# Kernel optimization log

Hardware: AMD Instinct MI355X
Metric: run time of the kernel (lower is better)

## Reference

```python
import jax, jax.numpy as jnp
import numpy as np

B, S, DIM = 2, 2048, 4096
NH, NKV, HD = 32, 8, 128
N_REP = NH // NKV


def setup_inputs() -> dict:
    key = jax.random.key(0)
    ks = jax.random.split(key, 6)
    scale = 0.02
    x = jax.random.normal(ks[0], (B, S, DIM), dtype=jnp.float32)
    # RoPE table: angles[s, i] = s / 10000^(2i/HD); stored as (cos, sin) pairs
    inv_freq = 1.0 / (10000.0 ** (np.arange(0, HD, 2, dtype=np.float32) / HD))
    ang = np.arange(S, dtype=np.float32)[:, None] * inv_freq[None, :]  # [S, HD/2]
    freqs_cis = jnp.asarray(np.stack([np.cos(ang), np.sin(ang)], axis=-1), dtype=jnp.float32)
    wq = jax.random.normal(ks[1], (DIM, NH * HD), dtype=jnp.float32) * scale
    wk = jax.random.normal(ks[2], (DIM, NKV * HD), dtype=jnp.float32) * scale
    wv = jax.random.normal(ks[3], (DIM, NKV * HD), dtype=jnp.float32) * scale
    wo = jax.random.normal(ks[4], (NH * HD, DIM), dtype=jnp.float32) * scale
    return {"x": x, "freqs_cis": freqs_cis, "wq": wq, "wk": wk, "wv": wv, "wo": wo}


def _apply_rope(xh, fc):
    # xh: [B, S, H, HD]; fc: [S, HD/2, 2] (cos, sin). Pairs are consecutive dims
    # (matches torch view_as_complex on reshape(..., -1, 2)). Done in fp32.
    b, s, h, d = xh.shape
    xp = xh.astype(jnp.float32).reshape(b, s, h, d // 2, 2)
    cos = fc[:, None, :, 0]  # [S, 1, HD/2] -> broadcasts over batch & heads
    sin = fc[:, None, :, 1]
    xr, xi = xp[..., 0], xp[..., 1]
    out_r = xr * cos - xi * sin
    out_i = xr * sin + xi * cos
    return jnp.stack([out_r, out_i], axis=-1).reshape(b, s, h, d).astype(xh.dtype)


def reference(x, freqs_cis, wq, wk, wv, wo):
    b, s, _ = x.shape
    xq = (x @ wq).reshape(b, s, NH, HD)
    xk = (x @ wk).reshape(b, s, NKV, HD)
    xv = (x @ wv).reshape(b, s, NKV, HD)
    xq = _apply_rope(xq, freqs_cis)
    xk = _apply_rope(xk, freqs_cis)
    new_k, new_v = xk, xv  # kv_cache is None -> new cache is this step's K/V

    # GQA: group query heads [NH] as [NKV, N_REP]; no K/V materialized repeat.
    q = xq.transpose(0, 2, 1, 3).reshape(b, NKV, N_REP, s, HD)
    k = xk.transpose(0, 2, 1, 3)  # [B, NKV, S, HD]
    v = xv.transpose(0, 2, 1, 3)
    scores = jnp.einsum("bgrqd,bgkd->bgrqk", q, k) / jnp.sqrt(jnp.float32(HD))
    attn = jax.nn.softmax(scores, axis=-1)  # is_causal=False -> full attention
    ctx = jnp.einsum("bgrqk,bgkd->bgrqd", attn, v)  # [B, NKV, N_REP, S, HD]
    ctx = ctx.reshape(b, NH, s, HD).transpose(0, 2, 1, 3).reshape(b, s, NH * HD)
    out = ctx @ wo
    return out, new_k, new_v
```

## Files before the change

### kernel.cpp

```cpp
#include <hip/hip_runtime.h>
#include <hip/hip_bf16.h>
#include <math.h>

#define B_    2
#define S_    2048
#define DIM_  4096
#define NH_   32
#define NKV_  8
#define HD_   128
#define NREP_ 4

typedef __attribute__((ext_vector_type(8))) short bf16x8;
typedef __attribute__((ext_vector_type(4))) float floatx4;

__device__ __forceinline__ unsigned short f2bf(float f) {
    unsigned int u = __float_as_uint(f);
    unsigned int r = (u + 0x7FFFu + ((u >> 16) & 1u)) >> 16;
    return (unsigned short)r;
}
__device__ __forceinline__ float bf2f(unsigned short u) {
    return __uint_as_float((unsigned int)u << 16);
}
__device__ __forceinline__ void gload_lds16(const unsigned short* g, unsigned short* l) {
    __builtin_amdgcn_global_load_lds(
        (const __attribute__((address_space(1))) void*)g,
        (__attribute__((address_space(3))) void*)l, 16, 0, 0);
}

__global__ __launch_bounds__(256)
void convert_bf16(const float* __restrict__ in, unsigned short* __restrict__ out,
                  long long n) {
    long long i = ((long long)blockIdx.x * 256 + threadIdx.x) * 4;
    if (i >= n) return;
    const float4 v = *(const float4*)(in + i);
    ushort4 o;
    o.x = f2bf(v.x); o.y = f2bf(v.y); o.z = f2bf(v.z); o.w = f2bf(v.w);
    *(ushort4*)(out + i) = o;
}

__global__ __launch_bounds__(256)
void transpose_conv(const float* __restrict__ W, unsigned short* __restrict__ Wt,
                    int K, int N) {
    __shared__ unsigned short t[32][33];
    const int tx = threadIdx.x & 31, ty = threadIdx.x >> 5;
    const int n0 = blockIdx.x * 32, k0 = blockIdx.y * 32;
    for (int i = 0; i < 4; ++i)
        t[ty + i * 8][tx] = f2bf(W[(size_t)(k0 + ty + i * 8) * N + n0 + tx]);
    __syncthreads();
    for (int i = 0; i < 4; ++i)
        Wt[(size_t)(n0 + ty + i * 8) * K + k0 + tx] = t[tx][ty + i * 8];
}

template<bool OUT_BF16>
__global__ __launch_bounds__(256)
void gemm_bt(const unsigned short* __restrict__ A,
             const unsigned short* __restrict__ Bt,
             void* __restrict__ C, int M, int N, int K) {
    __shared__ unsigned short As[128 * 32];
    __shared__ unsigned short Bs[128 * 32];
    const int tid  = threadIdx.x;
    const int lane = tid & 63;
    const int wave = tid >> 6;
    const int l16  = lane & 15;
    const int quad = lane >> 4;
    const int tileM = blockIdx.x * 128, tileN = blockIdx.y * 128;
    const int waveM = (wave >> 1) * 64, waveN = (wave & 1) * 64;

    floatx4 acc[4][4] = {};

    const int r0 = tid >> 2, ko = (tid & 3) * 8;

    for (int k0 = 0; k0 < K; k0 += 32) {
        for (int p = 0; p < 2; ++p) {
            const int idx = p * 256 + tid;
            const int row = r0 + p * 64;
            gload_lds16(A  + (size_t)(tileM + row) * K + k0 + ko, &As[idx * 8]);
            gload_lds16(Bt + (size_t)(tileN + row) * K + k0 + ko, &Bs[idx * 8]);
        }
        __syncthreads();
        bf16x8 af[4], bfr[4];
        for (int i = 0; i < 4; ++i) {
            af[i]  = *(const bf16x8*)&As[(waveM + i * 16 + l16) * 32 + quad * 8];
            bfr[i] = *(const bf16x8*)&Bs[(waveN + i * 16 + l16) * 32 + quad * 8];
        }
        for (int mi = 0; mi < 4; ++mi)
            for (int ni = 0; ni < 4; ++ni)
                acc[mi][ni] = __builtin_amdgcn_mfma_f32_16x16x32_bf16(
                    af[mi], bfr[ni], acc[mi][ni], 0, 0, 0);
        __syncthreads();
    }
    for (int mi = 0; mi < 4; ++mi)
        for (int r = 0; r < 4; ++r) {
            const int row = tileM + waveM + mi * 16 + quad * 4 + r;
            for (int ni = 0; ni < 4; ++ni) {
                const int col = tileN + waveN + ni * 16 + l16;
                if (OUT_BF16)
                    ((unsigned short*)C)[(size_t)row * N + col] = f2bf(acc[mi][ni][r]);
                else
                    ((float*)C)[(size_t)row * N + col] = acc[mi][ni][r];
            }
        }
}

__global__ __launch_bounds__(256)
void rope2(unsigned short* __restrict__ qio, const float* __restrict__ xk,
           const float* __restrict__ nv, const float* __restrict__ fc,
           unsigned short* __restrict__ kb, unsigned short* __restrict__ vtb,
           float* __restrict__ new_k) {
    const long long QP = (long long)B_ * S_ * NH_ * (HD_ / 2);
    const long long KP = (long long)B_ * S_ * NKV_ * (HD_ / 2);
    const long long idx = (long long)blockIdx.x * 256 + threadIdx.x;
    if (idx < QP) {
        const int d2 = (int)(idx & 63);
        const long long rh = idx >> 6;
        const int s = (int)((rh / NH_) % S_);
        const ushort2 u = *(const ushort2*)(qio + idx * 2);
        const float xr = bf2f(u.x), xi = bf2f(u.y);
        const float cs = fc[((size_t)s * 64 + d2) * 2];
        const float sn = fc[((size_t)s * 64 + d2) * 2 + 1];
        *(ushort2*)(qio + idx * 2) =
            make_ushort2(f2bf(xr * cs - xi * sn), f2bf(xr * sn + xi * cs));
    } else if (idx < QP + KP) {
        const long long e = idx - QP;
        const int d2 = (int)(e & 63);
        const long long rh = e >> 6;
        const int g = (int)(rh & (NKV_ - 1));
        const long long row = rh >> 3;
        const int b = (int)(row / S_), s = (int)(row % S_);
        const float2 v = *(const float2*)(xk + e * 2);
        const float cs = fc[((size_t)s * 64 + d2) * 2];
        const float sn = fc[((size_t)s * 64 + d2) * 2 + 1];
        const float orr = v.x * cs - v.y * sn;
        const float oii = v.x * sn + v.y * cs;
        *(float2*)(new_k + e * 2) = make_float2(orr, oii);
        const size_t kbi = ((size_t)(b * NKV_ + g) * S_ + s) * HD_ + d2 * 2;
        *(ushort2*)(kb + kbi) = make_ushort2(f2bf(orr), f2bf(oii));
    } else if (idx < QP + 2 * KP) {
        const long long e = idx - QP - KP;
        const float2 v = *(const float2*)(nv + e * 2);
        const long long fe = e * 2;
        const int c = (int)(fe & (HD_ - 1));
        const long long rh = fe >> 7;
        const int g = (int)(rh & (NKV_ - 1));
        const long long row = rh >> 3;
        const int b = (int)(row / S_), s = (int)(row % S_);
        const size_t base = ((size_t)(b * NKV_ + g) * HD_ + c) * S_ + s;
        vtb[base]      = f2bf(v.x);
        vtb[base + S_] = f2bf(v.y);
    }
}

__global__ __launch_bounds__(256)
void flash_attn(const unsigned short* __restrict__ qb,
                const unsigned short* __restrict__ kb,
                const unsigned short* __restrict__ vtb,
                unsigned short* __restrict__ ctxb) {
    __shared__ unsigned short Ks[2][64 * 128];
    __shared__ unsigned short Vs[2][128 * 64];
    __shared__ unsigned short Plds[4][16 * 72];
    const int tid  = threadIdx.x;
    const int wave = tid >> 6, lane = tid & 63;
    const int l16  = lane & 15, quad = lane >> 4;
    const int bi  = blockIdx.x;
    const int qt4 = bi & (S_ / 64 - 1);
    const int bh  = bi >> 5;
    const int h = bh & (NH_ - 1), b = bh >> 5;
    const int g = h >> 2;
    const int qt = qt4 * 4 + wave;
    const float scale = 0.08838834764831845f;

    const unsigned short* kbase = kb  + (size_t)(b * NKV_ + g) * S_ * HD_;
    const unsigned short* vbase = vtb + (size_t)(b * NKV_ + g) * HD_ * S_;

    bf16x8 qf[4];
    {
        const unsigned short* qp =
            qb + ((size_t)(b * S_ + qt * 16 + l16) * NH_ + h) * HD_;
        for (int c = 0; c < 4; ++c) qf[c] = *(const bf16x8*)(qp + c * 32 + quad * 8);
    }

    float m_i[4], l_i[4];
    for (int r = 0; r < 4; ++r) { m_i[r] = -1e30f; l_i[r] = 0.f; }
    floatx4 oacc[8] = {};
    unsigned short* pw = &Plds[wave][0];

    auto stage = [&](int buf, int kt) {
        for (int rnd = 0; rnd < 4; ++rnd) {
            const int ci = rnd * 256 + tid;
            const int row = ci >> 4, c = ci & 15;
            gload_lds16(kbase + (size_t)(kt + row) * HD_ + (c ^ (row & 15)) * 8,
                        &Ks[buf][ci * 8]);
        }
        for (int rnd = 0; rnd < 4; ++rnd) {
            const int ci = rnd * 256 + tid;
            const int row = ci >> 3, c = ci & 7;
            gload_lds16(vbase + (size_t)row * S_ + kt + (c ^ (row & 7)) * 8,
                        &Vs[buf][ci * 8]);
        }
    };

    stage(0, 0);
    __syncthreads();

    int cur = 0;
    for (int kt = 0; kt < S_; kt += 64) {
        if (kt + 64 < S_) stage(cur ^ 1, kt + 64);
        floatx4 sacc[4] = {};
        for (int t = 0; t < 4; ++t) {
            const int row = t * 16 + l16;
            const char* kp = (const char*)&Ks[cur][row * 128];
            for (int c = 0; c < 4; ++c) {
                const bf16x8 kf = *(const bf16x8*)
                    (kp + ((c * 64 + quad * 16) ^ (l16 << 4)));
                sacc[t] = __builtin_amdgcn_mfma_f32_16x16x32_bf16(qf[c], kf, sacc[t], 0, 0, 0);
            }
        }
        float alpha[4];
        for (int r = 0; r < 4; ++r) {
            const float s0 = sacc[0][r] * scale, s1 = sacc[1][r] * scale;
            const float s2 = sacc[2][r] * scale, s3 = sacc[3][r] * scale;
            float mx = fmaxf(fmaxf(s0, s1), fmaxf(s2, s3));
            for (int off = 1; off < 16; off <<= 1) mx = fmaxf(mx, __shfl_xor(mx, off));
            const float mnew = fmaxf(m_i[r], mx);
            const float a  = __expf(m_i[r] - mnew);
            const float e0 = __expf(s0 - mnew), e1 = __expf(s1 - mnew);
            const float e2 = __expf(s2 - mnew), e3 = __expf(s3 - mnew);
            float rs = (e0 + e1) + (e2 + e3);
            for (int off = 1; off < 16; off <<= 1) rs += __shfl_xor(rs, off);
            l_i[r] = l_i[r] * a + rs;
            m_i[r] = mnew;
            alpha[r] = a;
            const int ro = (quad * 4 + r) * 72 + l16;
            pw[ro]      = f2bf(e0);
            pw[ro + 16] = f2bf(e1);
            pw[ro + 32] = f2bf(e2);
            pw[ro + 48] = f2bf(e3);
        }
        for (int f = 0; f < 8; ++f)
            for (int r = 0; r < 4; ++r) oacc[f][r] *= alpha[r];
        asm volatile("s_waitcnt lgkmcnt(0)" ::: "memory");
        for (int t2 = 0; t2 < 2; ++t2) {
            const bf16x8 pf = *(const bf16x8*)&pw[l16 * 72 + t2 * 32 + quad * 8];
            for (int f = 0; f < 8; ++f) {
                const int row = f * 16 + l16;
                const bf16x8 vf = *(const bf16x8*)((const char*)&Vs[cur][row * 64]
                                   + ((t2 * 64 + quad * 16) ^ ((l16 & 7) << 4)));
                oacc[f] = __builtin_amdgcn_mfma_f32_16x16x32_bf16(pf, vf, oacc[f], 0, 0, 0);
            }
        }
        __syncthreads();
        cur ^= 1;
    }
    for (int r = 0; r < 4; ++r) {
        const float inv = 1.0f / l_i[r];
        const int srow = qt * 16 + quad * 4 + r;
        unsigned short* cp = ctxb + ((size_t)(b * S_ + srow) * NH_ + h) * HD_ + l16;
        for (int f = 0; f < 8; ++f) cp[f * 16] = f2bf(oacc[f][r] * inv);
    }
}

extern "C" void kernel_launch(void* const* d_in, const int* in_sizes, int n_in,
                              void* d_out, int out_size, void* d_ws, size_t ws_size,
                              hipStream_t stream) {
    const float* x  = (const float*)d_in[0];
    const float* fc = (const float*)d_in[1];
    const float* wq = (const float*)d_in[2];
    const float* wk = (const float*)d_in[3];
    const float* wv = (const float*)d_in[4];
    const float* wo = (const float*)d_in[5];

    float* out   = (float*)d_out;
    float* new_k = out + (size_t)B_ * S_ * NH_ * HD_;
    float* new_v = new_k + (size_t)B_ * S_ * NKV_ * HD_;

    char* ws = (char*)d_ws;
    unsigned short* xb   = (unsigned short*)(ws);
    unsigned short* wqT  = (unsigned short*)(ws + (32ull  << 20));
    unsigned short* wkT  = (unsigned short*)(ws + (64ull  << 20));
    unsigned short* wvT  = (unsigned short*)(ws + (72ull  << 20));
    unsigned short* xqb  = (unsigned short*)(ws + (80ull  << 20));
    float*          xk   = (float*)         (ws + (112ull << 20));
    unsigned short* kbuf = (unsigned short*)(ws + (128ull << 20));
    unsigned short* vtb  = (unsigned short*)(ws + (136ull << 20));
    unsigned short* ctxb = xb;
    unsigned short* woT  = wqT;

    const int M = B_ * S_;
    dim3 blk(256);

    convert_bf16<<<(int)(((size_t)M * DIM_ / 4 + 255) / 256), blk, 0, stream>>>(
        x, xb, (long long)M * DIM_);
    transpose_conv<<<dim3(DIM_ / 32, DIM_ / 32), blk, 0, stream>>>(wq, wqT, DIM_, DIM_);
    transpose_conv<<<dim3((NKV_ * HD_) / 32, DIM_ / 32), blk, 0, stream>>>(wk, wkT, DIM_, NKV_ * HD_);
    transpose_conv<<<dim3((NKV_ * HD_) / 32, DIM_ / 32), blk, 0, stream>>>(wv, wvT, DIM_, NKV_ * HD_);

    gemm_bt<true ><<<dim3(M / 128, (NH_  * HD_) / 128), blk, 0, stream>>>(xb, wqT, xqb,   M, NH_  * HD_, DIM_);
    gemm_bt<false><<<dim3(M / 128, (NKV_ * HD_) / 128), blk, 0, stream>>>(xb, wkT, xk,    M, NKV_ * HD_, DIM_);
    gemm_bt<false><<<dim3(M / 128, (NKV_ * HD_) / 128), blk, 0, stream>>>(xb, wvT, new_v, M, NKV_ * HD_, DIM_);

    transpose_conv<<<dim3(DIM_ / 32, DIM_ / 32), blk, 0, stream>>>(wo, woT, DIM_, DIM_);

    const long long totalPairs = (long long)B_ * S_ * (HD_ / 2) * (NH_ + 2 * NKV_);
    rope2<<<(int)((totalPairs + 255) / 256), blk, 0, stream>>>(
        xqb, xk, new_v, fc, kbuf, vtb, new_k);

    flash_attn<<<B_ * NH_ * (S_ / 64), blk, 0, stream>>>(xqb, kbuf, vtb, ctxb);

    gemm_bt<false><<<dim3(M / 128, DIM_ / 128), blk, 0, stream>>>(ctxb, woT, out, M, DIM_, DIM_);
}
```

Before: 1.202 ms.

## Streamline flash-attention softmax with exp2, lazy rescale, DPP row max, deferred sum

Rewrites the online-softmax inner loop of the attention kernel. The log2(e) factor is folded into the score scale so the kernel can use the native exp2. The row max now uses DPP row shifts instead of shuffles. The row sum stays per-lane and is reduced only once at the end. Rescaling of the running max and output is skipped when the new max stays within a threshold of the old one. It also packs the bf16 conversion with v_cvt_pk_bf16 and raises wave priority around the MFMA blocks. All of this targets VALU and cross-lane overhead between the two matmuls, at the cost of a divergent branch and a bounded growth of the unnormalised exponentials.

```diff
diff --git a/kernel.cpp b/kernel.cpp
--- a/kernel.cpp
+++ b/kernel.cpp
@@ -20,6 +20,23 @@
 }
 __device__ __forceinline__ float bf2f(unsigned short u) {
     return __uint_as_float((unsigned int)u << 16);
+}
+__device__ __forceinline__ unsigned int cvt_pk_bf16(float lo, float hi) {
+    unsigned int r;
+    asm("v_cvt_pk_bf16_f32 %0, %1, %2" : "=v"(r) : "v"(lo), "v"(hi));
+    return r;
+}
+__device__ __forceinline__ float rowmax16(float x) {
+    int t;
+    t = __builtin_amdgcn_mov_dpp(__float_as_int(x), 0x121, 0xf, 0xf, true);
+    x = fmaxf(x, __int_as_float(t));
+    t = __builtin_amdgcn_mov_dpp(__float_as_int(x), 0x122, 0xf, 0xf, true);
+    x = fmaxf(x, __int_as_float(t));
+    t = __builtin_amdgcn_mov_dpp(__float_as_int(x), 0x124, 0xf, 0xf, true);
+    x = fmaxf(x, __int_as_float(t));
+    t = __builtin_amdgcn_mov_dpp(__float_as_int(x), 0x128, 0xf, 0xf, true);
+    x = fmaxf(x, __int_as_float(t));
+    return x;
 }
 __device__ __forceinline__ void gload_lds16(const unsigned short* g, unsigned short* l) {
     __builtin_amdgcn_global_load_lds(
@@ -167,7 +184,7 @@
     const int h = bh & (NH_ - 1), b = bh >> 5;
     const int g = h >> 2;
     const int qt = qt4 * 4 + wave;
-    const float scale = 0.08838834764831845f;
+    const float sc2 = 0.12754857629633723f;
 
     const unsigned short* kbase = kb  + (size_t)(b * NKV_ + g) * S_ * HD_;
     const unsigned short* vbase = vtb + (size_t)(b * NKV_ + g) * HD_ * S_;
@@ -179,8 +196,8 @@
         for (int c = 0; c < 4; ++c) qf[c] = *(const bf16x8*)(qp + c * 32 + quad * 8);
     }
 
-    float m_i[4], l_i[4];
-    for (int r = 0; r < 4; ++r) { m_i[r] = -1e30f; l_i[r] = 0.f; }
+    float m_i[4], l_p[4];
+    for (int r = 0; r < 4; ++r) { m_i[r] = -1e30f; l_p[r] = 0.f; }
     floatx4 oacc[8] = {};
     unsigned short* pw = &Plds[wave][0];
 
@@ -206,6 +223,7 @@
     for (int kt = 0; kt < S_; kt += 64) {
         if (kt + 64 < S_) stage(cur ^ 1, kt + 64);
         floatx4 sacc[4] = {};
+        __builtin_amdgcn_s_setprio(1);
         for (int t = 0; t < 4; ++t) {
             const int row = t * 16 + l16;
             const char* kp = (const char*)&Ks[cur][row * 128];
@@ -215,30 +233,56 @@
                 sacc[t] = __builtin_amdgcn_mfma_f32_16x16x32_bf16(qf[c], kf, sacc[t], 0, 0, 0);
             }
         }
-        float alpha[4];
+        __builtin_amdgcn_s_setprio(0);
+        float sv[4][4], mx[4];
         for (int r = 0; r < 4; ++r) {
-            const float s0 = sacc[0][r] * scale, s1 = sacc[1][r] * scale;
-            const float s2 = sacc[2][r] * scale, s3 = sacc[3][r] * scale;
-            float mx = fmaxf(fmaxf(s0, s1), fmaxf(s2, s3));
-            for (int off = 1; off < 16; off <<= 1) mx = fmaxf(mx, __shfl_xor(mx, off));
-            const float mnew = fmaxf(m_i[r], mx);
-            const float a  = __expf(m_i[r] - mnew);
-            const float e0 = __expf(s0 - mnew), e1 = __expf(s1 - mnew);
-            const float e2 = __expf(s2 - mnew), e3 = __expf(s3 - mnew);
-            float rs = (e0 + e1) + (e2 + e3);
-            for (int off = 1; off < 16; off <<= 1) rs += __shfl_xor(rs, off);
-            l_i[r] = l_i[r] * a + rs;
-            m_i[r] = mnew;
-            alpha[r] = a;
-            const int ro = (quad * 4 + r) * 72 + l16;
-            pw[ro]      = f2bf(e0);
-            pw[ro + 16] = f2bf(e1);
-            pw[ro + 32] = f2bf(e2);
-            pw[ro + 48] = f2bf(e3);
-        }
-        for (int f = 0; f < 8; ++f)
-            for (int r = 0; r < 4; ++r) oacc[f][r] *= alpha[r];
+            const float s0 = sacc[0][r] * sc2, s1 = sacc[1][r] * sc2;
+            const float s2 = sacc[2][r] * sc2, s3 = sacc[3][r] * sc2;
+            sv[0][r] = s0; sv[1][r] = s1; sv[2][r] = s2; sv[3][r] = s3;
+            mx[r] = rowmax16(fmaxf(fmaxf(s0, s1), fmaxf(s2, s3)));
+        }
+        const bool ok = (mx[0] <= m_i[0] + 8.f) && (mx[1] <= m_i[1] + 8.f) &&
+                        (mx[2] <= m_i[2] + 8.f) && (mx[3] <= m_i[3] + 8.f);
+        if (__all(ok)) {
+            for (int r = 0; r < 4; ++r) {
+                const float e0 = __builtin_amdgcn_exp2f(sv[0][r] - m_i[r]);
+                const float e1 = __builtin_amdgcn_exp2f(sv[1][r] - m_i[r]);
+                const float e2 = __builtin_amdgcn_exp2f(sv[2][r] - m_i[r]);
+                const float e3 = __builtin_amdgcn_exp2f(sv[3][r] - m_i[r]);
+                l_p[r] += (e0 + e1) + (e2 + e3);
+                const int ro = (quad * 4 + r) * 72 + l16;
+                const unsigned int p01 = cvt_pk_bf16(e0, e1);
+                const unsigned int p23 = cvt_pk_bf16(e2, e3);
+                pw[ro]      = (unsigned short)p01;
+                pw[ro + 16] = (unsigned short)(p01 >> 16);
+                pw[ro + 32] = (unsigned short)p23;
+                pw[ro + 48] = (unsigned short)(p23 >> 16);
+            }
+        } else {
+            float alpha[4];
+            for (int r = 0; r < 4; ++r) {
+                const float mnew = fmaxf(m_i[r], mx[r]);
+                const float a  = __builtin_amdgcn_exp2f(m_i[r] - mnew);
+                const float e0 = __builtin_amdgcn_exp2f(sv[0][r] - mnew);
+                const float e1 = __builtin_amdgcn_exp2f(sv[1][r] - mnew);
+                const float e2 = __builtin_amdgcn_exp2f(sv[2][r] - mnew);
+                const float e3 = __builtin_amdgcn_exp2f(sv[3][r] - mnew);
+                l_p[r] = l_p[r] * a + (e0 + e1) + (e2 + e3);
+                m_i[r] = mnew;
+                alpha[r] = a;
+                const int ro = (quad * 4 + r) * 72 + l16;
+                const unsigned int p01 = cvt_pk_bf16(e0, e1);
+                const unsigned int p23 = cvt_pk_bf16(e2, e3);
+                pw[ro]      = (unsigned short)p01;
+                pw[ro + 16] = (unsigned short)(p01 >> 16);
+                pw[ro + 32] = (unsigned short)p23;
+                pw[ro + 48] = (unsigned short)(p23 >> 16);
+            }
+            for (int f = 0; f < 8; ++f)
+                for (int r = 0; r < 4; ++r) oacc[f][r] *= alpha[r];
+        }
         asm volatile("s_waitcnt lgkmcnt(0)" ::: "memory");
+        __builtin_amdgcn_s_setprio(1);
         for (int t2 = 0; t2 < 2; ++t2) {
             const bf16x8 pf = *(const bf16x8*)&pw[l16 * 72 + t2 * 32 + quad * 8];
             for (int f = 0; f < 8; ++f) {
@@ -248,11 +292,14 @@
                 oacc[f] = __builtin_amdgcn_mfma_f32_16x16x32_bf16(pf, vf, oacc[f], 0, 0, 0);
             }
         }
+        __builtin_amdgcn_s_setprio(0);
         __syncthreads();
         cur ^= 1;
     }
     for (int r = 0; r < 4; ++r) {
-        const float inv = 1.0f / l_i[r];
+        float l = l_p[r];
+        for (int off = 1; off < 16; off <<= 1) l += __shfl_xor(l, off);
+        const float inv = 1.0f / l;
         const int srow = qt * 16 + quad * 4 + r;
         unsigned short* cp = ctxb + ((size_t)(b * S_ + srow) * NH_ + h) * HD_ + l16;
         for (int f = 0; f < 8; ++f) cp[f * 16] = f2bf(oacc[f][r] * inv);
```

Measured after the change: 1.138 ms. 1.06x faster.
